# Optimization experiments

Hardware: AMD Instinct MI355X
Metric: run time of the kernel (lower is better)

Reference implementation:

```python
import jax, jax.numpy as jnp
import numpy as np

HEAD = 2

def setup_inputs() -> dict:
    key = jax.random.key(0)
    ks = jax.random.split(key, 12)
    B, C, H, W = 4, 512, 64, 64
    IC = 256
    N = H * W
    s = 0.02
    return {
        "x": jax.random.normal(ks[0], (B, C, H, W), jnp.float32),
        "output_attn": jax.random.normal(ks[1], (B, C, H, W), jnp.float32),
        "mlp_w": jax.random.normal(ks[2], (N, N), jnp.float32) * s,
        "mlp_b": jax.random.normal(ks[3], (N,), jnp.float32) * s,
        "g_w": jax.random.normal(ks[4], (IC, C), jnp.float32) * s,
        "g_b": jax.random.normal(ks[5], (IC,), jnp.float32) * s,
        "theta_w": jax.random.normal(ks[6], (IC, C), jnp.float32) * s,
        "theta_b": jax.random.normal(ks[7], (IC,), jnp.float32) * s,
        "phi_w": jax.random.normal(ks[8], (IC, C), jnp.float32) * s,
        "phi_b": jax.random.normal(ks[9], (IC,), jnp.float32) * s,
        "out_w": jax.random.normal(ks[10], (C, IC), jnp.float32) * s,
        "out_b": jax.random.normal(ks[11], (C,), jnp.float32) * s,
    }

def _conv1x1(feat, w, b):
    # feat: [B, Cin, N], w: [Cout, Cin], b: [Cout] -> [B, Cout, N]
    return jnp.einsum('bcn,oc->bon', feat, w) + b[None, :, None]

def reference(x, output_attn, mlp_w, mlp_b, g_w, g_b, theta_w, theta_b,
              phi_w, phi_b, out_w, out_b):
    B, C, H, W = x.shape
    N = H * W
    IC = g_w.shape[0]
    d = IC // HEAD  # per-head dim

    xf = x.reshape(B, C, N)
    # head-MLP remix: only hd==HEAD slice is non-empty (integer-division bug in source)
    xf = xf + (jnp.einsum('bcn,mn->bcm', xf, mlp_w) + mlp_b)

    g = _conv1x1(xf, g_w, g_b)                       # [B, IC, N]
    g = g.reshape(B * HEAD, d, N).transpose(0, 2, 1)  # [BH, N, d]

    oa = output_attn.reshape(B, C, N)
    th = _conv1x1(oa, theta_w, theta_b).reshape(B * HEAD, d, N).transpose(0, 2, 1)  # [BH, N, d]
    ph = _conv1x1(xf, phi_w, phi_b).reshape(B * HEAD, d, N)                          # [BH, d, N]

    scale = 1.0 / (d ** 0.5)
    attn = jax.nn.softmax(jnp.einsum('bnd,bdm->bnm', th, ph) * scale, axis=-1)  # [BH, N, N]
    y = jnp.einsum('bnm,bmd->bnd', attn, g)           # [BH, N, d]
    y = y.reshape(B, HEAD, N, d).transpose(0, 2, 1, 3).reshape(B, N, IC)
    y = y.transpose(0, 2, 1)                          # [B, IC, N]

    out = output_attn + _conv1x1(y, out_w, out_b).reshape(B, C, H, W)
    return out
```

## Files before the change

kernel.cpp:

```cpp
#include <hip/hip_runtime.h>

typedef unsigned short us;
typedef us s8v __attribute__((ext_vector_type(8)));
typedef us s4v __attribute__((ext_vector_type(4)));
typedef float f4v __attribute__((ext_vector_type(4)));
typedef __bf16 b2v __attribute__((ext_vector_type(2)));

static __device__ __forceinline__ us f2b(float f) {
  return __builtin_bit_cast(us, (__bf16)f);
}
static __device__ __forceinline__ unsigned f2b2(float lo, float hi) {
  b2v v = {(__bf16)lo, (__bf16)hi};
  return __builtin_bit_cast(unsigned, v);
}
static __device__ __forceinline__ float b2f(us s) {
  unsigned u = ((unsigned)s) << 16;
  return __builtin_bit_cast(float, u);
}

#define GLDS(src, dst)                                                        \
  __builtin_amdgcn_global_load_lds(                                           \
      (const __attribute__((address_space(1))) unsigned int*)(src),           \
      (__attribute__((address_space(3))) unsigned int*)(dst), 16, 0, 0)

__global__ __launch_bounds__(256) void castk(const float* __restrict__ in,
                                             us* __restrict__ out, int n4) {
  int i = blockIdx.x * 256 + threadIdx.x;
  int stride = gridDim.x * 256;
  for (; i < n4; i += stride) {
    float4 v = ((const float4*)in)[i];
    s4v s = {f2b(v.x), f2b(v.y), f2b(v.z), f2b(v.w)};
    ((s4v*)out)[i] = s;
  }
}

__global__ __launch_bounds__(256) void wcast4(const float* __restrict__ s0, us* __restrict__ o0,
                                              const float* __restrict__ s1, us* __restrict__ o1,
                                              const float* __restrict__ s2, us* __restrict__ o2,
                                              const float* __restrict__ s3, us* __restrict__ o3) {
  const float* s; us* o;
  int y = blockIdx.y;
  if (y == 0) { s = s0; o = o0; }
  else if (y == 1) { s = s1; o = o1; }
  else if (y == 2) { s = s2; o = o2; }
  else { s = s3; o = o3; }
  int i = blockIdx.x * 256 + threadIdx.x;
  for (; i < 32768; i += 8192) {
    float4 v = ((const float4*)s)[i];
    s4v r = {f2b(v.x), f2b(v.y), f2b(v.z), f2b(v.w)};
    ((s4v*)o)[i] = r;
  }
}

__global__ __launch_bounds__(256) void tcast(const float* __restrict__ in,
                                             us* __restrict__ out, int R, int C) {
  __shared__ float t[64][65];
  const int tid = threadIdx.x;
  const long r0 = (long)blockIdx.y * 64, c0 = (long)blockIdx.x * 64;
#pragma unroll
  for (int j = 0; j < 4; ++j) {
    int idx = j * 256 + tid;
    int row = idx >> 4, c4 = (idx & 15) * 4;
    float4 v = *(const float4*)(in + (r0 + row) * C + c0 + c4);
    t[row][c4] = v.x; t[row][c4 + 1] = v.y; t[row][c4 + 2] = v.z; t[row][c4 + 3] = v.w;
  }
  __syncthreads();
#pragma unroll
  for (int j = 0; j < 4; ++j) {
    int idx = j * 256 + tid;
    int orow = idx >> 4, r4 = (idx & 15) * 4;
    s4v s = {f2b(t[r4][orow]), f2b(t[r4 + 1][orow]), f2b(t[r4 + 2][orow]), f2b(t[r4 + 3][orow])};
    *(s4v*)(out + (c0 + orow) * R + r0 + r4) = s;
  }
}

#define SW(row, kb) ((row) * 128 + ((kb) ^ (((row) & 7) << 4)))

template <int EPI, int AF32, int BF32, int SWZ>
__global__ __launch_bounds__(256) void gemm_nt(
    const void* __restrict__ Av, const void* __restrict__ Bv,
    int lda, int ldb, int K, long aZ, long bZ,
    const float* __restrict__ bias,
    const us* __restrict__ addb16,
    const float* __restrict__ addf32,
    us* __restrict__ outb16,
    float* __restrict__ outf32) {
  __shared__ __align__(16) us lA[128 * 64];
  __shared__ __align__(16) us lB[128 * 64];
  const int tid = threadIdx.x, l = tid & 63;
  const int lr = l & 15, lg = l >> 4;
  const int w = tid >> 6, wr = w >> 1, wc = w & 1;
  int bm, bn;
  if constexpr (SWZ) {
    int flat = blockIdx.y * gridDim.x + blockIdx.x;
    int re = (flat & 7) * ((gridDim.x * gridDim.y) >> 3) + (flat >> 3);
    bm = re % gridDim.x; bn = re / gridDim.x;
  } else { bm = blockIdx.x; bn = blockIdx.y; }
  const int z = blockIdx.z;
  const f4v zero = {0.f, 0.f, 0.f, 0.f};
  f4v acc[4][4];
#pragma unroll
  for (int i = 0; i < 4; ++i)
#pragma unroll
    for (int j = 0; j < 4; ++j) acc[i][j] = zero;
  char* lab = (char*)lA;
  char* lbb = (char*)lB;

  for (int k0 = 0; k0 < K; k0 += 64) {
#pragma unroll
    for (int j = 0; j < 4; ++j) {
      int byte = j * 4096 + tid * 16;
      int row = byte >> 7, kb = byte & 127;
      if constexpr (AF32) {
        const float* af = (const float*)Av + (long)z * aZ + (long)(bm * 128 + row) * lda + k0 + (kb >> 1);
        float4 v0 = *(const float4*)af, v1 = *(const float4*)(af + 4);
        s8v va = {f2b(v0.x), f2b(v0.y), f2b(v0.z), f2b(v0.w), f2b(v1.x), f2b(v1.y), f2b(v1.z), f2b(v1.w)};
        *(s8v*)(lab + SW(row, kb)) = va;
      } else {
        s8v va = *(const s8v*)((const char*)Av + ((long)z * aZ + (long)(bm * 128 + row) * lda + k0) * 2 + kb);
        *(s8v*)(lab + SW(row, kb)) = va;
      }
      if constexpr (BF32) {
        const float* bf_ = (const float*)Bv + (long)z * bZ + (long)(bn * 128 + row) * ldb + k0 + (kb >> 1);
        float4 v0 = *(const float4*)bf_, v1 = *(const float4*)(bf_ + 4);
        s8v vb = {f2b(v0.x), f2b(v0.y), f2b(v0.z), f2b(v0.w), f2b(v1.x), f2b(v1.y), f2b(v1.z), f2b(v1.w)};
        *(s8v*)(lbb + SW(row, kb)) = vb;
      } else {
        s8v vb = *(const s8v*)((const char*)Bv + ((long)z * bZ + (long)(bn * 128 + row) * ldb + k0) * 2 + kb);
        *(s8v*)(lbb + SW(row, kb)) = vb;
      }
    }
    __syncthreads();
#pragma unroll
    for (int ks = 0; ks < 2; ++ks) {
      s8v af[4], bf[4];
      const int kb = ks * 64 + lg * 16;
#pragma unroll
      for (int mi = 0; mi < 4; ++mi) {
        int row = wr * 64 + mi * 16 + lr;
        af[mi] = *(const s8v*)(lab + SW(row, kb));
      }
#pragma unroll
      for (int ni = 0; ni < 4; ++ni) {
        int row = wc * 64 + ni * 16 + lr;
        bf[ni] = *(const s8v*)(lbb + SW(row, kb));
      }
#pragma unroll
      for (int mi = 0; mi < 4; ++mi)
#pragma unroll
        for (int ni = 0; ni < 4; ++ni)
          acc[mi][ni] = __builtin_amdgcn_mfma_f32_16x16x32_bf16(af[mi], bf[ni], acc[mi][ni], 0, 0, 0);
    }
    __syncthreads();
  }

#pragma unroll
  for (int mi = 0; mi < 4; ++mi) {
#pragma unroll
    for (int ni = 0; ni < 4; ++ni) {
#pragma unroll
      for (int r = 0; r < 4; ++r) {
        int row = bm * 128 + wr * 64 + mi * 16 + lg * 4 + r;
        int col = bn * 128 + wc * 64 + ni * 16 + lr;
        float v = acc[mi][ni][r];
        if constexpr (EPI == 0) {
          long idx = (long)row * 2048 + col;
          outb16[idx] = f2b(v + b2f(addb16[idx]) + bias[row]);
        } else if constexpr (EPI == 1) {
          long idx = ((long)(z * 2 + (col >> 7)) * 4096 + row) * 128 + (col & 127);
          outb16[idx] = f2b(v + bias[col]);
        } else if constexpr (EPI == 2) {
          long idx = ((long)(z * 256 + row)) * 4096 + col;
          outb16[idx] = f2b(v + bias[row]);
        } else {
          long idx = ((long)(z * 512 + row)) * 4096 + col;
          outf32[idx] = v + bias[row] + addf32[idx];
        }
      }
    }
  }
}

__global__ __launch_bounds__(256) void attn_k(const us* __restrict__ th,
                                              const us* __restrict__ pht,
                                              const us* __restrict__ g,
                                              us* __restrict__ yt) {
  __shared__ __align__(16) us ph2[2][64 * 128];
  __shared__ __align__(16) us g2[2][128 * 64];
  __shared__ __align__(16) us plds[4][1024];
  const int tid = threadIdx.x, l = tid & 63, w = tid >> 6;
  const int lr = l & 15, lg = l >> 4;
  const int flat = blockIdx.y * 64 + blockIdx.x;
  const int bh = flat & 7, qb = flat >> 3;
  const int b = bh >> 1, head = bh & 1;
  const float C1 = 0.12751802f;
  const f4v zero = {0.f, 0.f, 0.f, 0.f};

  const char* phsrc = (const char*)(pht + (long)bh * 4096 * 128);
  const char* gsrc = (const char*)(g + (long)(b * 256 + head * 128) * 4096);

  int koff[4], voff[4];
#pragma unroll
  for (int j = 0; j < 4; ++j) {
    int d = j * 4096 + tid * 16;
    koff[j] = d ^ (((d >> 8) & 7) << 4);
    int rowg = d >> 7, kbg = d & 127;
    voff[j] = rowg * 8192 + (kbg ^ ((rowg & 7) << 4));
  }

  s8v a_th[4];
  {
    const us* thp = th + ((long)bh * 4096 + qb * 64 + w * 16 + lr) * 128 + lg * 8;
#pragma unroll
    for (int ks = 0; ks < 4; ++ks) a_th[ks] = *(const s8v*)(thp + ks * 32);
  }
  f4v acc_y[8];
#pragma unroll
  for (int i = 0; i < 8; ++i) acc_y[i] = zero;
  float m_run = -1e30f, l_run = 0.f;
  char* pw = (char*)&plds[w][0];

  auto stage = [&](int bufi, int mt2) {
    char* dk = (char*)ph2[bufi] + w * 1024;
    char* dv = (char*)g2[bufi] + w * 1024;
    const char* sk = phsrc + (long)mt2 * 16384;
    const char* sv = gsrc + (long)mt2 * 128;
#pragma unroll
    for (int j = 0; j < 4; ++j) {
      GLDS(sk + koff[j], dk + j * 4096);
      GLDS(sv + voff[j], dv + j * 4096);
    }
  };

  stage(0, 0);
  __syncthreads();

  for (int mt = 0; mt < 64; ++mt) {
    const int cur = mt & 1;
    stage(cur ^ 1, (mt + 1) & 63);
    const char* phb = (const char*)ph2[cur];
    const char* gb = (const char*)g2[cur];

    f4v s_[4];
#pragma unroll
    for (int ct = 0; ct < 4; ++ct) s_[ct] = zero;
    __builtin_amdgcn_s_setprio(1);
#pragma unroll
    for (int ks = 0; ks < 4; ++ks) {
      const int kb = ks * 64 + lg * 16;
#pragma unroll
      for (int ct = 0; ct < 4; ++ct) {
        int row = ct * 16 + lr;
        s8v kf = *(const s8v*)(phb + row * 256 + (kb ^ ((row & 7) << 4)));
        s_[ct] = __builtin_amdgcn_mfma_f32_16x16x32_bf16(kf, a_th[ks], s_[ct], 0, 0, 0);
      }
    }
    __builtin_amdgcn_s_setprio(0);

    float m0 = fmaxf(fmaxf(s_[0][0], s_[0][1]), fmaxf(s_[0][2], s_[0][3]));
    float m1 = fmaxf(fmaxf(s_[1][0], s_[1][1]), fmaxf(s_[1][2], s_[1][3]));
    float m2 = fmaxf(fmaxf(s_[2][0], s_[2][1]), fmaxf(s_[2][2], s_[2][3]));
    float m3 = fmaxf(fmaxf(s_[3][0], s_[3][1]), fmaxf(s_[3][2], s_[3][3]));
    float mx = fmaxf(fmaxf(m0, m1), fmaxf(m2, m3));
    mx = fmaxf(mx, __shfl_xor(mx, 16, 64));
    mx = fmaxf(mx, __shfl_xor(mx, 32, 64));

    if (__any(mx > m_run + 60.0f)) {
      float mn = fmaxf(m_run, mx);
      float corr = __builtin_amdgcn_exp2f((m_run - mn) * C1);
      m_run = mn;
      l_run *= corr;
      float cb0 = __shfl(corr, lg * 4 + 0, 64);
      float cb1 = __shfl(corr, lg * 4 + 1, 64);
      float cb2 = __shfl(corr, lg * 4 + 2, 64);
      float cb3 = __shfl(corr, lg * 4 + 3, 64);
#pragma unroll
      for (int dt = 0; dt < 8; ++dt) {
        acc_y[dt][0] *= cb0; acc_y[dt][1] *= cb1;
        acc_y[dt][2] *= cb2; acc_y[dt][3] *= cb3;
      }
    }

    const float nmsc = -m_run * C1;
    float sum = 0.f;
    unsigned pk[8];
#pragma unroll
    for (int ct = 0; ct < 4; ++ct) {
      float p0 = __builtin_amdgcn_exp2f(__builtin_fmaf(s_[ct][0], C1, nmsc));
      float p1 = __builtin_amdgcn_exp2f(__builtin_fmaf(s_[ct][1], C1, nmsc));
      float p2 = __builtin_amdgcn_exp2f(__builtin_fmaf(s_[ct][2], C1, nmsc));
      float p3 = __builtin_amdgcn_exp2f(__builtin_fmaf(s_[ct][3], C1, nmsc));
      sum += (p0 + p1) + (p2 + p3);
      pk[ct * 2] = f2b2(p0, p1);
      pk[ct * 2 + 1] = f2b2(p2, p3);
    }
    sum += __shfl_xor(sum, 16, 64);
    sum += __shfl_xor(sum, 32, 64);
    l_run += sum;

#pragma unroll
    for (int ct = 0; ct < 4; ++ct) {
      uint2 v; v.x = pk[ct * 2]; v.y = pk[ct * 2 + 1];
      *(uint2*)(pw + lr * 128 + ((ct * 32 + lg * 8) ^ ((lr & 7) << 4))) = v;
    }

#pragma unroll
    for (int ks2 = 0; ks2 < 2; ++ks2) {
      const int kb = ks2 * 64 + lg * 16;
      s8v ap = *(const s8v*)(pw + lr * 128 + (kb ^ ((lr & 7) << 4)));
      __builtin_amdgcn_s_setprio(1);
#pragma unroll
      for (int dt = 0; dt < 8; ++dt) {
        int row = lr + 16 * dt;
        s8v bg = *(const s8v*)(gb + SW(row, kb));
        acc_y[dt] = __builtin_amdgcn_mfma_f32_16x16x32_bf16(ap, bg, acc_y[dt], 0, 0, 0);
      }
      __builtin_amdgcn_s_setprio(0);
    }

    __syncthreads();
  }

  float inv = 1.0f / l_run;
  float i0 = __shfl(inv, lg * 4 + 0, 64);
  float i1 = __shfl(inv, lg * 4 + 1, 64);
  float i2 = __shfl(inv, lg * 4 + 2, 64);
  float i3 = __shfl(inv, lg * 4 + 3, 64);
  float iv[4] = {i0, i1, i2, i3};
#pragma unroll
  for (int r = 0; r < 4; ++r) {
    long n = (long)qb * 64 + w * 16 + lg * 4 + r;
    us* dst = yt + ((long)b * 4096 + n) * 256 + head * 128 + lr;
#pragma unroll
    for (int dt = 0; dt < 8; ++dt) dst[dt * 16] = f2b(acc_y[dt][r] * iv[r]);
  }
}

extern "C" void kernel_launch(void* const* d_in, const int* in_sizes, int n_in,
                              void* d_out, int out_size, void* d_ws, size_t ws_size,
                              hipStream_t stream) {
  (void)in_sizes; (void)n_in; (void)out_size;
  const float* x       = (const float*)d_in[0];
  const float* oa      = (const float*)d_in[1];
  const float* mlp_w   = (const float*)d_in[2];
  const float* mlp_b   = (const float*)d_in[3];
  const float* g_w     = (const float*)d_in[4];
  const float* g_b     = (const float*)d_in[5];
  const float* theta_w = (const float*)d_in[6];
  const float* theta_b = (const float*)d_in[7];
  const float* phi_w   = (const float*)d_in[8];
  const float* phi_b   = (const float*)d_in[9];
  const float* out_w   = (const float*)d_in[10];
  const float* out_b   = (const float*)d_in[11];
  float* out = (float*)d_out;
  char* ws = (char*)d_ws;

  us* xf_t   = (us*)(ws + 0L);
  us* oat    = (us*)(ws + 16777216L);
  us* xt     = (us*)(ws + 33554432L);
  us* g_ws   = (us*)(ws + 33554432L);
  us* th_ws  = (us*)(ws + 41943040L);
  us* xc     = (us*)(ws + 50331648L);
  us* ph_ws  = (us*)(ws + 50331648L);
  us* yt     = (us*)(ws + 58720256L);
  us* g_wb   = (us*)(ws + 67108864L);
  us* th_wb  = (us*)(ws + 67371008L);
  us* ph_wb  = (us*)(ws + 67633152L);
  us* out_wb = (us*)(ws + 67895296L);
  us* mlp_wb = (us*)(ws + 68157440L);
  const bool big = ws_size >= 101711872ULL;

  wcast4<<<dim3(32, 4), dim3(256), 0, stream>>>(g_w, g_wb, theta_w, th_wb,
                                                phi_w, ph_wb, out_w, out_wb);
  castk<<<dim3(1024), dim3(256), 0, stream>>>(x, xc, 2097152);
  tcast<<<dim3(64, 32), dim3(256), 0, stream>>>(x, xt, 2048, 4096);
  tcast<<<dim3(64, 32), dim3(256), 0, stream>>>(oa, oat, 2048, 4096);

  if (big) {
    castk<<<dim3(1024), dim3(256), 0, stream>>>(mlp_w, mlp_wb, 4194304);
    gemm_nt<0, 0, 0, 1><<<dim3(32, 16, 1), dim3(256), 0, stream>>>(
        mlp_wb, xc, 4096, 4096, 4096, 0, 0, mlp_b, xt, nullptr, xf_t, nullptr);
  } else {
    gemm_nt<0, 1, 0, 1><<<dim3(32, 16, 1), dim3(256), 0, stream>>>(
        mlp_w, xc, 4096, 4096, 4096, 0, 0, mlp_b, xt, nullptr, xf_t, nullptr);
  }

  gemm_nt<1, 0, 0, 0><<<dim3(32, 2, 4), dim3(256), 0, stream>>>(
      oat, th_wb, 2048, 512, 512, 512, 0, theta_b, nullptr, nullptr, th_ws, nullptr);
  gemm_nt<1, 0, 0, 0><<<dim3(32, 2, 4), dim3(256), 0, stream>>>(
      xf_t, ph_wb, 2048, 512, 512, 512, 0, phi_b, nullptr, nullptr, ph_ws, nullptr);
  gemm_nt<2, 0, 0, 0><<<dim3(2, 32, 4), dim3(256), 0, stream>>>(
      g_wb, xf_t, 512, 2048, 512, 0, 512, g_b, nullptr, nullptr, g_ws, nullptr);

  attn_k<<<dim3(64, 8), dim3(256), 0, stream>>>(th_ws, ph_ws, g_ws, yt);

  gemm_nt<3, 0, 0, 0><<<dim3(4, 32, 4), dim3(256), 0, stream>>>(
      out_wb, yt, 256, 256, 256, 0, 1048576L, out_b, nullptr, oa, nullptr, out);
}
```

Measured before the change: 306.9 us.

## Use 32x32 MFMA with register-resident P and split-KV attention merge

The attention kernel switches to 32x32x16 MFMA tiles so each wave handles 32 query rows. It builds the P operand in registers through permlane32 swaps instead of a round trip through LDS. The key range is split into two halves across blocks, with the grid kept at 512 blocks and a launch-bounds occupancy hint. Each half writes partial outputs plus max/sum values, and a new merge kernel combines them. This removes LDS traffic for P and raises MFMA efficiency, at the cost of an extra kernel launch and partial-result memory traffic in bf16.

```diff
diff --git a/kernel.cpp b/kernel.cpp
--- a/kernel.cpp
+++ b/kernel.cpp
@@ -4,6 +4,7 @@
 typedef us s8v __attribute__((ext_vector_type(8)));
 typedef us s4v __attribute__((ext_vector_type(4)));
 typedef float f4v __attribute__((ext_vector_type(4)));
+typedef float f16v __attribute__((ext_vector_type(16)));
 typedef __bf16 b2v __attribute__((ext_vector_type(2)));
 
 static __device__ __forceinline__ us f2b(float f) {
@@ -181,20 +182,23 @@
   }
 }
 
-__global__ __launch_bounds__(256) void attn_k(const us* __restrict__ th,
-                                              const us* __restrict__ pht,
-                                              const us* __restrict__ g,
-                                              us* __restrict__ yt) {
+__global__ __launch_bounds__(256, 2) void attn_k(const us* __restrict__ th,
+                                                 const us* __restrict__ pht,
+                                                 const us* __restrict__ g,
+                                                 us* __restrict__ pY,
+                                                 float2* __restrict__ pml) {
   __shared__ __align__(16) us ph2[2][64 * 128];
   __shared__ __align__(16) us g2[2][128 * 64];
-  __shared__ __align__(16) us plds[4][1024];
   const int tid = threadIdx.x, l = tid & 63, w = tid >> 6;
-  const int lr = l & 15, lg = l >> 4;
-  const int flat = blockIdx.y * 64 + blockIdx.x;
-  const int bh = flat & 7, qb = flat >> 3;
+  const int l31 = l & 31, h = l >> 5;
+  const int swz = (l & 7) << 4;
+  const int flat = blockIdx.y * 32 + blockIdx.x;
+  const int bh = flat & 7, rest = flat >> 3;
+  const int half = rest & 1, qb = rest >> 1;
   const int b = bh >> 1, head = bh & 1;
+  const int m00 = half * 2048;
   const float C1 = 0.12751802f;
-  const f4v zero = {0.f, 0.f, 0.f, 0.f};
+  const f16v zero16 = {0.f};
 
   const char* phsrc = (const char*)(pht + (long)bh * 4096 * 128);
   const char* gsrc = (const char*)(g + (long)(b * 256 + head * 128) * 4096);
@@ -208,23 +212,21 @@
     voff[j] = rowg * 8192 + (kbg ^ ((rowg & 7) << 4));
   }
 
-  s8v a_th[4];
+  s8v qf[8];
   {
-    const us* thp = th + ((long)bh * 4096 + qb * 64 + w * 16 + lr) * 128 + lg * 8;
-#pragma unroll
-    for (int ks = 0; ks < 4; ++ks) a_th[ks] = *(const s8v*)(thp + ks * 32);
-  }
-  f4v acc_y[8];
-#pragma unroll
-  for (int i = 0; i < 8; ++i) acc_y[i] = zero;
+    const us* thp = th + ((long)bh * 4096 + qb * 128 + w * 32 + l31) * 128 + h * 8;
+#pragma unroll
+    for (int ks = 0; ks < 8; ++ks) qf[ks] = *(const s8v*)(thp + ks * 16);
+  }
+
+  f16v acc0 = zero16, acc1 = zero16, acc2 = zero16, acc3 = zero16;
   float m_run = -1e30f, l_run = 0.f;
-  char* pw = (char*)&plds[w][0];
-
-  auto stage = [&](int bufi, int mt2) {
+
+  auto stage = [&](int bufi, int m0) {
     char* dk = (char*)ph2[bufi] + w * 1024;
     char* dv = (char*)g2[bufi] + w * 1024;
-    const char* sk = phsrc + (long)mt2 * 16384;
-    const char* sv = gsrc + (long)mt2 * 128;
+    const char* sk = phsrc + (long)m0 * 256;
+    const char* sv = gsrc + (long)m0 * 2;
 #pragma unroll
     for (int j = 0; j < 4; ++j) {
       GLDS(sk + koff[j], dk + j * 4096);
@@ -232,37 +234,34 @@
     }
   };
 
-  stage(0, 0);
+  stage(0, m00);
   __syncthreads();
 
-  for (int mt = 0; mt < 64; ++mt) {
-    const int cur = mt & 1;
-    stage(cur ^ 1, (mt + 1) & 63);
+  for (int t = 0; t < 32; ++t) {
+    const int cur = t & 1;
+    stage(cur ^ 1, m00 + ((t + 1) & 31) * 64);
     const char* phb = (const char*)ph2[cur];
     const char* gb = (const char*)g2[cur];
 
-    f4v s_[4];
-#pragma unroll
-    for (int ct = 0; ct < 4; ++ct) s_[ct] = zero;
+    f16v sA[2] = {zero16, zero16};
     __builtin_amdgcn_s_setprio(1);
 #pragma unroll
-    for (int ks = 0; ks < 4; ++ks) {
-      const int kb = ks * 64 + lg * 16;
-#pragma unroll
-      for (int ct = 0; ct < 4; ++ct) {
-        int row = ct * 16 + lr;
-        s8v kf = *(const s8v*)(phb + row * 256 + (kb ^ ((row & 7) << 4)));
-        s_[ct] = __builtin_amdgcn_mfma_f32_16x16x32_bf16(kf, a_th[ks], s_[ct], 0, 0, 0);
-      }
+    for (int ks = 0; ks < 8; ++ks) {
+      const int kb = (ks * 32) ^ swz;
+#pragma unroll
+      for (int mt = 0; mt < 2; ++mt) {
+        s8v kf = *(const s8v*)(phb + (mt * 32 + l31) * 256 + (((ks * 32) + h * 16) ^ swz));
+        sA[mt] = __builtin_amdgcn_mfma_f32_32x32x16_bf16(kf, qf[ks], sA[mt], 0, 0, 0);
+      }
+      (void)kb;
     }
     __builtin_amdgcn_s_setprio(0);
 
-    float m0 = fmaxf(fmaxf(s_[0][0], s_[0][1]), fmaxf(s_[0][2], s_[0][3]));
-    float m1 = fmaxf(fmaxf(s_[1][0], s_[1][1]), fmaxf(s_[1][2], s_[1][3]));
-    float m2 = fmaxf(fmaxf(s_[2][0], s_[2][1]), fmaxf(s_[2][2], s_[2][3]));
-    float m3 = fmaxf(fmaxf(s_[3][0], s_[3][1]), fmaxf(s_[3][2], s_[3][3]));
-    float mx = fmaxf(fmaxf(m0, m1), fmaxf(m2, m3));
-    mx = fmaxf(mx, __shfl_xor(mx, 16, 64));
+    float mx = sA[0][0];
+#pragma unroll
+    for (int r = 1; r < 16; ++r) mx = fmaxf(mx, sA[0][r]);
+#pragma unroll
+    for (int r = 0; r < 16; ++r) mx = fmaxf(mx, sA[1][r]);
     mx = fmaxf(mx, __shfl_xor(mx, 32, 64));
 
     if (__any(mx > m_run + 60.0f)) {
@@ -270,70 +269,102 @@
       float corr = __builtin_amdgcn_exp2f((m_run - mn) * C1);
       m_run = mn;
       l_run *= corr;
-      float cb0 = __shfl(corr, lg * 4 + 0, 64);
-      float cb1 = __shfl(corr, lg * 4 + 1, 64);
-      float cb2 = __shfl(corr, lg * 4 + 2, 64);
-      float cb3 = __shfl(corr, lg * 4 + 3, 64);
-#pragma unroll
-      for (int dt = 0; dt < 8; ++dt) {
-        acc_y[dt][0] *= cb0; acc_y[dt][1] *= cb1;
-        acc_y[dt][2] *= cb2; acc_y[dt][3] *= cb3;
-      }
-    }
-
-    const float nmsc = -m_run * C1;
+#pragma unroll
+      for (int r = 0; r < 16; ++r) {
+        acc0[r] *= corr; acc1[r] *= corr; acc2[r] *= corr; acc3[r] *= corr;
+      }
+    }
+
+    const float nm = -m_run * C1;
     float sum = 0.f;
-    unsigned pk[8];
-#pragma unroll
-    for (int ct = 0; ct < 4; ++ct) {
-      float p0 = __builtin_amdgcn_exp2f(__builtin_fmaf(s_[ct][0], C1, nmsc));
-      float p1 = __builtin_amdgcn_exp2f(__builtin_fmaf(s_[ct][1], C1, nmsc));
-      float p2 = __builtin_amdgcn_exp2f(__builtin_fmaf(s_[ct][2], C1, nmsc));
-      float p3 = __builtin_amdgcn_exp2f(__builtin_fmaf(s_[ct][3], C1, nmsc));
-      sum += (p0 + p1) + (p2 + p3);
-      pk[ct * 2] = f2b2(p0, p1);
-      pk[ct * 2 + 1] = f2b2(p2, p3);
-    }
-    sum += __shfl_xor(sum, 16, 64);
+    s8v bfrag[4];
+#pragma unroll
+    for (int mt = 0; mt < 2; ++mt) {
+#pragma unroll
+      for (int k1 = 0; k1 < 2; ++k1) {
+        const int base = k1 * 8;
+        float p0 = __builtin_amdgcn_exp2f(__builtin_fmaf(sA[mt][base + 0], C1, nm));
+        float p1 = __builtin_amdgcn_exp2f(__builtin_fmaf(sA[mt][base + 1], C1, nm));
+        float p2 = __builtin_amdgcn_exp2f(__builtin_fmaf(sA[mt][base + 2], C1, nm));
+        float p3 = __builtin_amdgcn_exp2f(__builtin_fmaf(sA[mt][base + 3], C1, nm));
+        float p4 = __builtin_amdgcn_exp2f(__builtin_fmaf(sA[mt][base + 4], C1, nm));
+        float p5 = __builtin_amdgcn_exp2f(__builtin_fmaf(sA[mt][base + 5], C1, nm));
+        float p6 = __builtin_amdgcn_exp2f(__builtin_fmaf(sA[mt][base + 6], C1, nm));
+        float p7 = __builtin_amdgcn_exp2f(__builtin_fmaf(sA[mt][base + 7], C1, nm));
+        sum += ((p0 + p1) + (p2 + p3)) + ((p4 + p5) + (p6 + p7));
+        unsigned E0 = f2b2(p0, p1), E1 = f2b2(p2, p3);
+        unsigned O0 = f2b2(p4, p5), O1 = f2b2(p6, p7);
+        asm("v_permlane32_swap_b32 %0, %1" : "+v"(E0), "+v"(O0));
+        asm("v_permlane32_swap_b32 %0, %1" : "+v"(E1), "+v"(O1));
+        uint4 u = {E0, E1, O0, O1};
+        bfrag[mt * 2 + k1] = __builtin_bit_cast(s8v, u);
+      }
+    }
     sum += __shfl_xor(sum, 32, 64);
     l_run += sum;
 
-#pragma unroll
-    for (int ct = 0; ct < 4; ++ct) {
-      uint2 v; v.x = pk[ct * 2]; v.y = pk[ct * 2 + 1];
-      *(uint2*)(pw + lr * 128 + ((ct * 32 + lg * 8) ^ ((lr & 7) << 4))) = v;
-    }
-
-#pragma unroll
-    for (int ks2 = 0; ks2 < 2; ++ks2) {
-      const int kb = ks2 * 64 + lg * 16;
-      s8v ap = *(const s8v*)(pw + lr * 128 + (kb ^ ((lr & 7) << 4)));
-      __builtin_amdgcn_s_setprio(1);
-#pragma unroll
-      for (int dt = 0; dt < 8; ++dt) {
-        int row = lr + 16 * dt;
-        s8v bg = *(const s8v*)(gb + SW(row, kb));
-        acc_y[dt] = __builtin_amdgcn_mfma_f32_16x16x32_bf16(ap, bg, acc_y[dt], 0, 0, 0);
-      }
-      __builtin_amdgcn_s_setprio(0);
-    }
+    __builtin_amdgcn_s_setprio(1);
+#pragma unroll
+    for (int ks2 = 0; ks2 < 4; ++ks2) {
+      const int kb = ((ks2 * 32) + h * 16) ^ swz;
+      s8v v0 = *(const s8v*)(gb + (l31) * 128 + kb);
+      s8v v1 = *(const s8v*)(gb + (32 + l31) * 128 + kb);
+      s8v v2 = *(const s8v*)(gb + (64 + l31) * 128 + kb);
+      s8v v3 = *(const s8v*)(gb + (96 + l31) * 128 + kb);
+      acc0 = __builtin_amdgcn_mfma_f32_32x32x16_bf16(v0, bfrag[ks2], acc0, 0, 0, 0);
+      acc1 = __builtin_amdgcn_mfma_f32_32x32x16_bf16(v1, bfrag[ks2], acc1, 0, 0, 0);
+      acc2 = __builtin_amdgcn_mfma_f32_32x32x16_bf16(v2, bfrag[ks2], acc2, 0, 0, 0);
+      acc3 = __builtin_amdgcn_mfma_f32_32x32x16_bf16(v3, bfrag[ks2], acc3, 0, 0, 0);
+    }
+    __builtin_amdgcn_s_setprio(0);
 
     __syncthreads();
   }
 
-  float inv = 1.0f / l_run;
-  float i0 = __shfl(inv, lg * 4 + 0, 64);
-  float i1 = __shfl(inv, lg * 4 + 1, 64);
-  float i2 = __shfl(inv, lg * 4 + 2, 64);
-  float i3 = __shfl(inv, lg * 4 + 3, 64);
-  float iv[4] = {i0, i1, i2, i3};
-#pragma unroll
-  for (int r = 0; r < 4; ++r) {
-    long n = (long)qb * 64 + w * 16 + lg * 4 + r;
-    us* dst = yt + ((long)b * 4096 + n) * 256 + head * 128 + lr;
-#pragma unroll
-    for (int dt = 0; dt < 8; ++dt) dst[dt * 16] = f2b(acc_y[dt][r] * iv[r]);
-  }
+  const long gq = (long)bh * 4096 + qb * 128 + w * 32 + l31;
+  if (h == 0) pml[gq * 2 + half] = make_float2(m_run, l_run);
+  us* py = pY + (gq * 2 + half) * 128;
+#pragma unroll
+  for (int gi = 0; gi < 4; ++gi) {
+    int r0 = gi * 4;
+    {
+      uint2 u = {f2b2(acc0[r0], acc0[r0 + 1]), f2b2(acc0[r0 + 2], acc0[r0 + 3])};
+      *(uint2*)(py + gi * 8 + 4 * h) = u;
+    }
+    {
+      uint2 u = {f2b2(acc1[r0], acc1[r0 + 1]), f2b2(acc1[r0 + 2], acc1[r0 + 3])};
+      *(uint2*)(py + 32 + gi * 8 + 4 * h) = u;
+    }
+    {
+      uint2 u = {f2b2(acc2[r0], acc2[r0 + 1]), f2b2(acc2[r0 + 2], acc2[r0 + 3])};
+      *(uint2*)(py + 64 + gi * 8 + 4 * h) = u;
+    }
+    {
+      uint2 u = {f2b2(acc3[r0], acc3[r0 + 1]), f2b2(acc3[r0 + 2], acc3[r0 + 3])};
+      *(uint2*)(py + 96 + gi * 8 + 4 * h) = u;
+    }
+  }
+}
+
+__global__ __launch_bounds__(256) void mergek(const us* __restrict__ pY,
+                                              const float2* __restrict__ pml,
+                                              us* __restrict__ yt) {
+  const float C1 = 0.12751802f;
+  int idx = blockIdx.x * 256 + threadIdx.x;
+  int gq = idx >> 4, dd8 = (idx & 15) * 8;
+  float2 A = pml[gq * 2 + 0], B = pml[gq * 2 + 1];
+  float M = fmaxf(A.x, B.x);
+  float e0 = __builtin_amdgcn_exp2f((A.x - M) * C1);
+  float e1 = __builtin_amdgcn_exp2f((B.x - M) * C1);
+  float inv = 1.0f / (A.y * e0 + B.y * e1);
+  e0 *= inv; e1 *= inv;
+  s8v Y0 = *(const s8v*)(pY + ((long)gq * 2 + 0) * 128 + dd8);
+  s8v Y1 = *(const s8v*)(pY + ((long)gq * 2 + 1) * 128 + dd8);
+  s8v o;
+#pragma unroll
+  for (int i = 0; i < 8; ++i) o[i] = f2b(e0 * b2f(Y0[i]) + e1 * b2f(Y1[i]));
+  int bh = gq >> 12, q = gq & 4095, b = bh >> 1, head = bh & 1;
+  *(s8v*)(yt + ((long)b * 4096 + q) * 256 + head * 128 + dd8) = o;
 }
 
 extern "C" void kernel_launch(void* const* d_in, const int* in_sizes, int n_in,
@@ -356,7 +387,9 @@
   char* ws = (char*)d_ws;
 
   us* xf_t   = (us*)(ws + 0L);
+  us* pY     = (us*)(ws + 0L);
   us* oat    = (us*)(ws + 16777216L);
+  float2* pml = (float2*)(ws + 16777216L);
   us* xt     = (us*)(ws + 33554432L);
   us* g_ws   = (us*)(ws + 33554432L);
   us* th_ws  = (us*)(ws + 41943040L);
@@ -392,7 +425,8 @@
   gemm_nt<2, 0, 0, 0><<<dim3(2, 32, 4), dim3(256), 0, stream>>>(
       g_wb, xf_t, 512, 2048, 512, 0, 512, g_b, nullptr, nullptr, g_ws, nullptr);
 
-  attn_k<<<dim3(64, 8), dim3(256), 0, stream>>>(th_ws, ph_ws, g_ws, yt);
+  attn_k<<<dim3(32, 16), dim3(256), 0, stream>>>(th_ws, ph_ws, g_ws, pY, pml);
+  mergek<<<dim3(2048), dim3(256), 0, stream>>>(pY, pml, yt);
 
   gemm_nt<3, 0, 0, 0><<<dim3(4, 32, 4), dim3(256), 0, stream>>>(
       out_wb, yt, 256, 256, 256, 0, 1048576L, out_b, nullptr, oa, nullptr, out);
```

Result: faster. 280.3 us (-8.7%).
